# Kernel optimization log

Measured on AMD Instinct MI355X. Metric: run time of the kernel, lower is better.

The kernel has to match this reference:

```python
import jax, jax.numpy as jnp
import numpy as np

N_R, N_V, D, E_RR, L, G = 50000, 2000, 128, 800000, 3, 32


def setup_inputs() -> dict:
    key = jax.random.key(0)
    ks = jax.random.split(key, 10)
    x_real = jax.random.normal(ks[0], (N_R, D), dtype=jnp.float32)
    x_virtual = jax.random.normal(ks[1], (N_V, D), dtype=jnp.float32)
    # params: [num_layers, 3 relations (r_to_r, r_to_v, v_to_r), D, D]
    W_root = jax.random.normal(ks[2], (L, 3, D, D), dtype=jnp.float32) * 0.05
    W_nbr = jax.random.normal(ks[3], (L, 3, D, D), dtype=jnp.float32) * 0.05
    bias = jax.random.normal(ks[4], (L, 3, D), dtype=jnp.float32) * 0.05
    edge_rr = jax.random.randint(ks[5], (2, E_RR), 0, N_R)
    # one virtual-node edge per real node (hierarchical virtual nodes)
    src_rv = jnp.arange(N_R)
    dst_rv = jax.random.randint(ks[6], (N_R,), 0, N_V)
    edge_rv = jnp.stack([src_rv, dst_rv])          # real -> virtual
    edge_vr = jnp.stack([dst_rv, src_rv])          # virtual -> real
    batch_real = jnp.sort(jax.random.randint(ks[7], (N_R,), 0, G))
    return {
        "x_real": x_real, "x_virtual": x_virtual,
        "W_root": W_root, "W_nbr": W_nbr, "bias": bias,
        "edge_rr": edge_rr, "edge_rv": edge_rv, "edge_vr": edge_vr,
        "batch_real": batch_real,
    }


def _graph_conv(x_src, x_dst, src, dst, Wr, Wn, b, n_dst):
    # PyG GraphConv-style: root transform + sum-aggregated neighbor messages
    msg = jax.ops.segment_sum(x_src[src] @ Wn, dst, num_segments=n_dst)
    return x_dst @ Wr + msg + b


def _forward(x_real, x_virtual, W_root, W_nbr, bias, edge_rr, edge_rv, edge_vr, batch_real):
    x_r, x_v = x_real, x_virtual
    n_r, n_v = x_r.shape[0], x_v.shape[0]
    for l in range(W_root.shape[0]):
        # HeteroConv with aggr='sum': sum relation outputs per destination type
        c_rr = _graph_conv(x_r, x_r, edge_rr[0], edge_rr[1], W_root[l, 0], W_nbr[l, 0], bias[l, 0], n_r)
        c_vr = _graph_conv(x_v, x_r, edge_vr[0], edge_vr[1], W_root[l, 2], W_nbr[l, 2], bias[l, 2], n_r)
        c_rv = _graph_conv(x_r, x_v, edge_rv[0], edge_rv[1], W_root[l, 1], W_nbr[l, 1], bias[l, 1], n_v)
        # activation + dropout (eval mode -> identity)
        x_r = jax.nn.relu(c_rr + c_vr)
        x_v = jax.nn.relu(c_rv)
    # mean readout over real nodes per graph
    counts = jax.ops.segment_sum(jnp.ones((n_r,), x_r.dtype), batch_real, num_segments=G)
    graph_emb = jax.ops.segment_sum(x_r, batch_real, num_segments=G) / jnp.maximum(counts, 1.0)[:, None]
    return x_r, graph_emb


def reference(x_real, x_virtual, W_root, W_nbr, bias, edge_rr, edge_rv, edge_vr, batch_real):
    node_embedding, graph_embedding = _forward(
        x_real, x_virtual, W_root, W_nbr, bias, edge_rr, edge_rv, edge_vr, batch_real)
    return node_embedding, graph_embedding
```

## Files before the change

### kernel.cpp

```cpp
#include <hip/hip_runtime.h>
#include <hip/hip_bf16.h>

#define N_R   50000
#define N_V   2000
#define DIM   128
#define E_RR  800000
#define NLAY  3
#define NGR   32
#define RCHUNK 16

#define BUKD  128
#define NBUK  391
#define CHKE  2048
#define NCHK  391

typedef __attribute__((ext_vector_type(8))) short bf16x8;
typedef __attribute__((ext_vector_type(4))) float f32x4;
typedef __attribute__((ext_vector_type(8))) unsigned char u8x8;
typedef __attribute__((ext_vector_type(4))) unsigned char u8x4;

__device__ __forceinline__ ushort f2bf(float f) {
    unsigned u = __builtin_bit_cast(unsigned, f);
    unsigned r = (u + 0x7fffu + ((u >> 16) & 1u)) >> 16;
    return (ushort)r;
}
__device__ __forceinline__ float bf2f(ushort h) {
    unsigned u = ((unsigned)h) << 16;
    return __builtin_bit_cast(float, u);
}
__device__ __forceinline__ int lbound(const int* __restrict__ a, int n, int key) {
    int lo = 0, hi = n;
    while (lo < hi) { int mid = (lo + hi) >> 1; if (a[mid] < key) lo = mid + 1; else hi = mid; }
    return lo;
}

__global__ __launch_bounds__(256) void hist_kernel(
    const int* __restrict__ dst, int n, int* __restrict__ cnt)
{
    int i = blockIdx.x * 256 + threadIdx.x;
    if (i < n) atomicAdd(&cnt[dst[i]], 1);
}

__global__ __launch_bounds__(256) void scan_single_kernel(
    const int* __restrict__ cnt, int n, int nedges,
    int* __restrict__ rowptr, int* __restrict__ cursor)
{
    __shared__ int lds[256];
    __shared__ int carry;
    int t = threadIdx.x;
    if (t == 0) carry = 0;
    __syncthreads();
    for (int base = 0; base < n; base += 256) {
        int i = base + t;
        int v = (i < n) ? cnt[i] : 0;
        lds[t] = v;
        __syncthreads();
        #pragma unroll
        for (int off = 1; off < 256; off <<= 1) {
            int u = (t >= off) ? lds[t - off] : 0;
            __syncthreads();
            lds[t] += u;
            __syncthreads();
        }
        int excl = carry + lds[t] - v;
        if (i < n) {
            rowptr[i] = excl;
            if (cursor) cursor[i] = excl;
        }
        __syncthreads();
        if (t == 255) carry += lds[255];
        __syncthreads();
    }
    if (t == 0) rowptr[n] = nedges;
}

__global__ __launch_bounds__(256) void fill_kernel(
    const int* __restrict__ src, const int* __restrict__ dst, int n,
    int* __restrict__ cursor, int* __restrict__ col)
{
    int i = blockIdx.x * 256 + threadIdx.x;
    if (i < n) {
        int p = atomicAdd(&cursor[dst[i]], 1);
        col[p] = src[i];
    }
}

__global__ __launch_bounds__(256) void bkt_count_kernel(
    const int* __restrict__ dst, int* __restrict__ cnt2d)
{
    __shared__ int h[NBUK];
    int t = threadIdx.x, c = blockIdx.x;
    for (int i = t; i < NBUK; i += 256) h[i] = 0;
    __syncthreads();
    int e0 = c * CHKE, e1 = min(e0 + CHKE, E_RR);
    for (int e = e0 + t; e < e1; e += 256) atomicAdd(&h[dst[e] >> 7], 1);
    __syncthreads();
    for (int i = t; i < NBUK; i += 256) cnt2d[(size_t)c * NBUK + i] = h[i];
}

__global__ __launch_bounds__(64) void bkt_prefix_kernel(
    const int* __restrict__ cnt2d, int* __restrict__ rel2d, int* __restrict__ tot)
{
    int b = blockIdx.x, lane = threadIdx.x;
    int base = 0;
    for (int c0 = 0; c0 < NCHK; c0 += 64) {
        int c = c0 + lane;
        int v = (c < NCHK) ? cnt2d[(size_t)c * NBUK + b] : 0;
        int s = v;
        #pragma unroll
        for (int off = 1; off < 64; off <<= 1) {
            int u = __shfl_up(s, off);
            if (lane >= off) s += u;
        }
        if (c < NCHK) rel2d[(size_t)c * NBUK + b] = base + s - v;
        base += __shfl(s, 63);
    }
    if (lane == 0) tot[b] = base;
}

__global__ __launch_bounds__(256) void bkt_scatter_kernel(
    const int* __restrict__ src, const int* __restrict__ dst,
    const int* __restrict__ rel2d, const int* __restrict__ bstart,
    unsigned* __restrict__ ebuf)
{
    __shared__ int cur[NBUK];
    int t = threadIdx.x, c = blockIdx.x;
    for (int i = t; i < NBUK; i += 256)
        cur[i] = bstart[i] + rel2d[(size_t)c * NBUK + i];
    __syncthreads();
    int e0 = c * CHKE, e1 = min(e0 + CHKE, E_RR);
    for (int e = e0 + t; e < e1; e += 256) {
        int d = dst[e];
        int p = atomicAdd(&cur[d >> 7], 1);
        ebuf[p] = ((unsigned)d << 16) | (unsigned)src[e];
    }
}

__global__ __launch_bounds__(256) void bkt_fine_kernel(
    const unsigned* __restrict__ ebuf, const int* __restrict__ bstart,
    int* __restrict__ rowptr, int* __restrict__ col)
{
    __shared__ int cnt[BUKD];
    __shared__ int sc[BUKD];
    __shared__ int cur[BUKD];
    int b = blockIdx.x, t = threadIdx.x;
    int s0 = bstart[b], s1 = bstart[b + 1];
    if (t < BUKD) cnt[t] = 0;
    __syncthreads();
    for (int e = s0 + t; e < s1; e += 256)
        atomicAdd(&cnt[(ebuf[e] >> 16) & (BUKD - 1)], 1);
    __syncthreads();
    if (t < BUKD) sc[t] = cnt[t];
    __syncthreads();
    #pragma unroll
    for (int off = 1; off < BUKD; off <<= 1) {
        int v = (t < BUKD && t >= off) ? sc[t - off] : 0;
        __syncthreads();
        if (t < BUKD) sc[t] += v;
        __syncthreads();
    }
    if (t < BUKD) {
        int ex = sc[t] - cnt[t];
        int d = b * BUKD + t;
        if (d < N_R) rowptr[d] = s0 + ex;
        cur[t] = ex;
    }
    if (b == NBUK - 1 && t == 0) rowptr[N_R] = E_RR;
    __syncthreads();
    for (int e = s0 + t; e < s1; e += 256) {
        unsigned pk = ebuf[e];
        int p = atomicAdd(&cur[(pk >> 16) & (BUKD - 1)], 1);
        col[s0 + p] = (int)(pk & 0xffffu);
    }
}

__global__ __launch_bounds__(256) void quant_input_kernel(
    const float* __restrict__ in, unsigned char* __restrict__ q,
    float2* __restrict__ meta)
{
    int w = (blockIdx.x * 256 + threadIdx.x) >> 6;
    int lane = threadIdx.x & 63;
    if (w >= N_R) return;
    float2 v = *(const float2*)(in + (size_t)w * DIM + lane * 2);
    float mn = fminf(v.x, v.y), mx = fmaxf(v.x, v.y);
    #pragma unroll
    for (int off = 1; off < 64; off <<= 1) {
        mn = fminf(mn, __shfl_xor(mn, off));
        mx = fmaxf(mx, __shfl_xor(mx, off));
    }
    float range = mx - mn;
    float inv = (range > 0.f) ? 255.f / range : 0.f;
    unsigned q0 = (unsigned)__float2int_rn((v.x - mn) * inv);
    unsigned q1 = (unsigned)__float2int_rn((v.y - mn) * inv);
    *(ushort*)(q + (size_t)w * DIM + lane * 2) = (ushort)(q0 | (q1 << 8));
    if (lane == 0) meta[w] = make_float2(range / 255.f, mn);
}

__global__ __launch_bounds__(256) void build_wt_kernel(
    const float* __restrict__ Wroot, const float* __restrict__ Wnbr,
    ushort* __restrict__ WT)
{
    int idx = blockIdx.x * 256 + threadIdx.x;
    if (idx >= NLAY * DIM * 2 * DIM) return;
    int k = idx & 255;
    int n = (idx >> 8) & 127;
    int l = idx >> 15;
    float v;
    if (k < DIM) {
        const float* base = Wroot + (size_t)l * 3 * DIM * DIM;
        v = base[(size_t)k * DIM + n] + base[(size_t)(2 * DIM + k) * DIM + n];
    } else {
        v = Wnbr[((size_t)l * 3 * DIM + (k - DIM)) * DIM + n];
    }
    WT[idx] = f2bf(v);
}

__global__ __launch_bounds__(256) void combine_b_kernel(
    const float* __restrict__ bias, float* __restrict__ bc)
{
    int idx = blockIdx.x * 256 + threadIdx.x;
    if (idx >= NLAY * DIM) return;
    int l = idx / DIM;
    int rest = idx - l * DIM;
    const float* base = bias + (size_t)l * 3 * DIM;
    bc[idx] = base[rest] + base[2 * DIM + rest];
}

__global__ __launch_bounds__(128) void vlayer_kernel(
    const int* __restrict__ rowptr, const int* __restrict__ col,
    const unsigned char* __restrict__ Xq, const float2* __restrict__ Xm,
    const float* __restrict__ xv,
    const float* __restrict__ Wn2, const float* __restrict__ Wr1,
    const float* __restrict__ Wn1, const float* __restrict__ b1,
    float* __restrict__ Tv, float* __restrict__ xv_next, int doNext)
{
    __shared__ float arv_s[4 * DIM];
    int t = threadIdx.x;
    int lr = t >> 5;
    int j4 = (t & 31) << 2;
    int row = blockIdx.x * 4 + lr;

    if (doNext) {
        int beg = rowptr[row], end = rowptr[row + 1];
        float a0 = 0.f, a1 = 0.f, a2 = 0.f, a3 = 0.f, msum = 0.f;
        int e = beg;
        for (; e + 3 < end; e += 4) {
            int c0 = col[e + 0], c1 = col[e + 1], c2 = col[e + 2], c3 = col[e + 3];
            float2 m0 = Xm[c0], m1 = Xm[c1], m2 = Xm[c2], m3 = Xm[c3];
            u8x4 u0 = *(const u8x4*)(Xq + (size_t)c0 * DIM + j4);
            u8x4 u1 = *(const u8x4*)(Xq + (size_t)c1 * DIM + j4);
            u8x4 u2 = *(const u8x4*)(Xq + (size_t)c2 * DIM + j4);
            u8x4 u3 = *(const u8x4*)(Xq + (size_t)c3 * DIM + j4);
            a0 += m0.x * (float)u0[0] + m1.x * (float)u1[0] + m2.x * (float)u2[0] + m3.x * (float)u3[0];
            a1 += m0.x * (float)u0[1] + m1.x * (float)u1[1] + m2.x * (float)u2[1] + m3.x * (float)u3[1];
            a2 += m0.x * (float)u0[2] + m1.x * (float)u1[2] + m2.x * (float)u2[2] + m3.x * (float)u3[2];
            a3 += m0.x * (float)u0[3] + m1.x * (float)u1[3] + m2.x * (float)u2[3] + m3.x * (float)u3[3];
            msum += m0.y + m1.y + m2.y + m3.y;
        }
        for (; e < end; ++e) {
            int c0 = col[e];
            float2 m0 = Xm[c0];
            u8x4 u0 = *(const u8x4*)(Xq + (size_t)c0 * DIM + j4);
            a0 += m0.x * (float)u0[0];
            a1 += m0.x * (float)u0[1];
            a2 += m0.x * (float)u0[2];
            a3 += m0.x * (float)u0[3];
            msum += m0.y;
        }
        arv_s[lr * DIM + j4 + 0] = a0 + msum;
        arv_s[lr * DIM + j4 + 1] = a1 + msum;
        arv_s[lr * DIM + j4 + 2] = a2 + msum;
        arv_s[lr * DIM + j4 + 3] = a3 + msum;
        __syncthreads();
    }

    const float* arow = xv + (size_t)row * DIM;
    float4 tacc = make_float4(0.f, 0.f, 0.f, 0.f);
    float4 nacc = make_float4(0.f, 0.f, 0.f, 0.f);
    if (doNext) {
        #pragma unroll 4
        for (int k = 0; k < DIM; ++k) {
            float av = arow[k];
            float bv = arv_s[lr * DIM + k];
            float4 w2 = *(const float4*)(Wn2 + (size_t)k * DIM + j4);
            float4 wr = *(const float4*)(Wr1 + (size_t)k * DIM + j4);
            float4 wn = *(const float4*)(Wn1 + (size_t)k * DIM + j4);
            tacc.x += av * w2.x; tacc.y += av * w2.y;
            tacc.z += av * w2.z; tacc.w += av * w2.w;
            nacc.x += av * wr.x + bv * wn.x;
            nacc.y += av * wr.y + bv * wn.y;
            nacc.z += av * wr.z + bv * wn.z;
            nacc.w += av * wr.w + bv * wn.w;
        }
    } else {
        #pragma unroll 8
        for (int k = 0; k < DIM; ++k) {
            float av = arow[k];
            float4 w2 = *(const float4*)(Wn2 + (size_t)k * DIM + j4);
            tacc.x += av * w2.x; tacc.y += av * w2.y;
            tacc.z += av * w2.z; tacc.w += av * w2.w;
        }
    }
    *(float4*)(Tv + (size_t)row * DIM + j4) = tacc;
    if (doNext) {
        float4 b = *(const float4*)(b1 + j4);
        nacc.x = fmaxf(nacc.x + b.x, 0.f);
        nacc.y = fmaxf(nacc.y + b.y, 0.f);
        nacc.z = fmaxf(nacc.z + b.z, 0.f);
        nacc.w = fmaxf(nacc.w + b.w, 0.f);
        *(float4*)(xv_next + (size_t)row * DIM + j4) = nacc;
    }
}

__global__ __launch_bounds__(128) void fused_layer_kernel(
    const int* __restrict__ rowptr, const int* __restrict__ col,
    const unsigned char* __restrict__ Xq, const float2* __restrict__ Xm,
    const ushort* __restrict__ WT,
    const float* __restrict__ Tv,  const int* __restrict__ vmap,
    const float* __restrict__ bias,
    float* __restrict__ outF,
    unsigned char* __restrict__ Xq_out, float2* __restrict__ Xm_out, int M)
{
    __shared__ ushort a2[16 * DIM];
    __shared__ float ost[16 * DIM];
    int t = threadIdx.x;

    int wave = t >> 6, lane = t & 63;
    int rlo = lane & 15, hi = lane >> 4;
    int row0 = blockIdx.x * 16;
    int arowc = min(row0 + rlo, M - 1);
    float2 am = Xm[arowc];
    bf16x8 afr[8];
    #pragma unroll
    for (int j = 0; j < 4; ++j) {
        u8x8 uv = *(const u8x8*)(Xq + (size_t)arowc * DIM + 32 * j + 8 * hi);
        bf16x8 f;
        #pragma unroll
        for (int q = 0; q < 8; ++q)
            f[q] = (short)f2bf(am.x * (float)uv[q] + am.y);
        afr[j] = f;
    }
    int vr[4];
    #pragma unroll
    for (int i = 0; i < 4; ++i)
        vr[i] = vmap[min(row0 + 4 * hi + i, M - 1)];

    int g = t >> 4;
    int li = t & 15;
    for (int rr = g; rr < 16; rr += 8) {
        int drow = min(row0 + rr, M - 1);
        int beg = rowptr[drow], end = rowptr[drow + 1];
        float acc[8] = {0.f,0.f,0.f,0.f,0.f,0.f,0.f,0.f};
        float msum = 0.f;
        int e = beg;
        for (; e + 3 < end; e += 4) {
            int c0 = col[e + 0], c1 = col[e + 1], c2 = col[e + 2], c3 = col[e + 3];
            float2 m0 = Xm[c0], m1 = Xm[c1], m2 = Xm[c2], m3 = Xm[c3];
            u8x8 v0 = *(const u8x8*)(Xq + (size_t)c0 * DIM + li * 8);
            u8x8 v1 = *(const u8x8*)(Xq + (size_t)c1 * DIM + li * 8);
            u8x8 v2 = *(const u8x8*)(Xq + (size_t)c2 * DIM + li * 8);
            u8x8 v3 = *(const u8x8*)(Xq + (size_t)c3 * DIM + li * 8);
            #pragma unroll
            for (int q = 0; q < 8; ++q) {
                acc[q] += (m0.x * (float)v0[q] + m1.x * (float)v1[q])
                        + (m2.x * (float)v2[q] + m3.x * (float)v3[q]);
            }
            msum += (m0.y + m1.y) + (m2.y + m3.y);
        }
        for (; e < end; ++e) {
            int c0 = col[e];
            float2 m0 = Xm[c0];
            u8x8 v0 = *(const u8x8*)(Xq + (size_t)c0 * DIM + li * 8);
            #pragma unroll
            for (int q = 0; q < 8; ++q) acc[q] += m0.x * (float)v0[q];
            msum += m0.y;
        }
        bf16x8 pk;
        #pragma unroll
        for (int q = 0; q < 8; ++q) pk[q] = (short)f2bf(acc[q] + msum);
        int byte = rr * 256 + ((li * 16) ^ ((rr & 7) << 4));
        *(bf16x8*)((char*)a2 + byte) = pk;
    }
    __syncthreads();

    #pragma unroll
    for (int jj = 0; jj < 4; ++jj) {
        int byte = rlo * 256 + ((64 * jj + 16 * hi) ^ ((rlo & 7) << 4));
        afr[4 + jj] = *(const bf16x8*)((const char*)a2 + byte);
    }

    f32x4 acc[4];
    #pragma unroll
    for (int n = 0; n < 4; ++n) acc[n] = (f32x4){0.f, 0.f, 0.f, 0.f};

    #pragma unroll
    for (int n = 0; n < 4; ++n) {
        int nt = wave * 4 + n;
        const ushort* wrow = WT + (size_t)(nt * 16 + rlo) * (2 * DIM);
        #pragma unroll
        for (int j = 0; j < 8; ++j) {
            bf16x8 bfr = *(const bf16x8*)(wrow + 32 * j + 8 * hi);
            acc[n] = __builtin_amdgcn_mfma_f32_16x16x32_bf16(afr[j], bfr, acc[n], 0, 0, 0);
        }
    }

    if (outF) {
        #pragma unroll
        for (int n = 0; n < 4; ++n) {
            int ncol = (wave * 4 + n) * 16 + rlo;
            float bv = bias[ncol];
            #pragma unroll
            for (int i = 0; i < 4; ++i) {
                int orow = row0 + 4 * hi + i;
                if (orow >= M) continue;
                float v = acc[n][i] + bv + Tv[(size_t)vr[i] * DIM + ncol];
                outF[(size_t)orow * DIM + ncol] = fmaxf(v, 0.f);
            }
        }
    } else {
        #pragma unroll
        for (int n = 0; n < 4; ++n) {
            int ncol = (wave * 4 + n) * 16 + rlo;
            float bv = bias[ncol];
            #pragma unroll
            for (int i = 0; i < 4; ++i) {
                float v = acc[n][i] + bv + Tv[(size_t)vr[i] * DIM + ncol];
                ost[(4 * hi + i) * DIM + ncol] = fmaxf(v, 0.f);
            }
        }
        __syncthreads();
        for (int rr = g; rr < 16; rr += 8) {
            int orow = row0 + rr;
            float4 f0 = *(const float4*)(ost + rr * DIM + li * 8);
            float4 f1 = *(const float4*)(ost + rr * DIM + li * 8 + 4);
            float mn = fminf(fminf(fminf(f0.x, f0.y), fminf(f0.z, f0.w)),
                             fminf(fminf(f1.x, f1.y), fminf(f1.z, f1.w)));
            float mx = fmaxf(fmaxf(fmaxf(f0.x, f0.y), fmaxf(f0.z, f0.w)),
                             fmaxf(fmaxf(f1.x, f1.y), fmaxf(f1.z, f1.w)));
            #pragma unroll
            for (int off = 1; off < 16; off <<= 1) {
                mn = fminf(mn, __shfl_xor(mn, off, 16));
                mx = fmaxf(mx, __shfl_xor(mx, off, 16));
            }
            float range = mx - mn;
            float inv = (range > 0.f) ? 255.f / range : 0.f;
            if (orow < M) {
                u8x8 qv;
                qv[0] = (unsigned char)__float2int_rn((f0.x - mn) * inv);
                qv[1] = (unsigned char)__float2int_rn((f0.y - mn) * inv);
                qv[2] = (unsigned char)__float2int_rn((f0.z - mn) * inv);
                qv[3] = (unsigned char)__float2int_rn((f0.w - mn) * inv);
                qv[4] = (unsigned char)__float2int_rn((f1.x - mn) * inv);
                qv[5] = (unsigned char)__float2int_rn((f1.y - mn) * inv);
                qv[6] = (unsigned char)__float2int_rn((f1.z - mn) * inv);
                qv[7] = (unsigned char)__float2int_rn((f1.w - mn) * inv);
                *(u8x8*)(Xq_out + (size_t)orow * DIM + li * 8) = qv;
                if (li == 0) Xm_out[orow] = make_float2(range / 255.f, mn);
            }
        }
    }
}

__global__ __launch_bounds__(256) void readout_kernel(
    const float* __restrict__ xr, const int* __restrict__ batch,
    float* __restrict__ gsum, int nrows)
{
    __shared__ float lds[256 * 4];
    int g = blockIdx.x / RCHUNK;
    int chunk = blockIdx.x % RCHUNK;
    int lo = lbound(batch, nrows, g);
    int hi = lbound(batch, nrows, g + 1);
    int len = hi - lo;
    if (len == 0) return;
    int per = (len + RCHUNK - 1) / RCHUNK;
    int r0 = lo + chunk * per;
    int r1 = min(r0 + per, hi);

    int t = threadIdx.x;
    int c4 = (t & 31) << 2;
    int rsub = t >> 5;

    float4 acc = make_float4(0.f, 0.f, 0.f, 0.f);
    for (int r = r0 + rsub; r < r1; r += 8) {
        float4 v = *(const float4*)(xr + (size_t)r * DIM + c4);
        acc.x += v.x; acc.y += v.y; acc.z += v.z; acc.w += v.w;
    }
    *(float4*)(lds + t * 4) = acc;
    __syncthreads();
    if (rsub == 0) {
        float4 s = make_float4(0.f, 0.f, 0.f, 0.f);
        #pragma unroll
        for (int j = 0; j < 8; ++j) {
            float4 v = *(const float4*)(lds + (j * 32 + t) * 4);
            s.x += v.x; s.y += v.y; s.z += v.z; s.w += v.w;
        }
        atomicAdd(&gsum[(size_t)g * DIM + c4 + 0], s.x);
        atomicAdd(&gsum[(size_t)g * DIM + c4 + 1], s.y);
        atomicAdd(&gsum[(size_t)g * DIM + c4 + 2], s.z);
        atomicAdd(&gsum[(size_t)g * DIM + c4 + 3], s.w);
    }
}

__global__ __launch_bounds__(256) void finalize_kernel(
    const float* __restrict__ gsum, const int* __restrict__ batch,
    float* __restrict__ out, int nrows)
{
    int idx = blockIdx.x * 256 + threadIdx.x;
    if (idx >= NGR * DIM) return;
    int g = idx >> 7;
    int lo = lbound(batch, nrows, g);
    int hi = lbound(batch, nrows, g + 1);
    float c = fmaxf((float)(hi - lo), 1.f);
    out[idx] = gsum[idx] / c;
}

extern "C" void kernel_launch(void* const* d_in, const int* in_sizes, int n_in,
                              void* d_out, int out_size, void* d_ws, size_t ws_size,
                              hipStream_t stream)
{
    const float* x_real    = (const float*)d_in[0];
    const float* x_virtual = (const float*)d_in[1];
    const float* W_root    = (const float*)d_in[2];
    const float* W_nbr     = (const float*)d_in[3];
    const float* bias      = (const float*)d_in[4];
    const int*   edge_rr   = (const int*)d_in[5];
    const int*   edge_rv   = (const int*)d_in[6];
    const int*   edge_vr   = (const int*)d_in[7];
    const int*   batch     = (const int*)d_in[8];

    float* out = (float*)d_out;

    float2* meta0 = (float2*)d_ws;
    float2* meta1 = meta0 + N_R;
    float2* meta2 = meta1 + N_R;
    float*  Tv    = (float*)(meta2 + N_R);
    float*  xv_a  = Tv   + (size_t)N_V * DIM;
    float*  xv_b  = xv_a + (size_t)N_V * DIM;
    float*  bc    = xv_b + (size_t)N_V * DIM;
    float*  gsum  = bc   + (size_t)NLAY * DIM;
    ushort* WT    = (ushort*)(gsum + NGR * DIM);
    int* iws       = (int*)(WT + (size_t)NLAY * DIM * 2 * DIM);
    int* rowptr_rr = iws;
    int* col_rr    = rowptr_rr + N_R + 1;
    int* cnt_v     = col_rr + E_RR;
    int* rowptr_rv = cnt_v + N_V;
    int* cursor_rv = rowptr_rv + N_V + 1;
    int* col_rv    = cursor_rv + N_V;
    int* cnt2d     = col_rv + N_R;
    int* rel2d     = cnt2d + NCHK * NBUK;
    int* tot       = rel2d + NCHK * NBUK;
    int* bstart    = tot + NBUK;
    unsigned* ebuf = (unsigned*)(bstart + NBUK + 1);
    unsigned char* Q0 = (unsigned char*)(ebuf + E_RR);
    unsigned char* Q1 = Q0 + (size_t)N_R * DIM;
    unsigned char* Q2 = Q1 + (size_t)N_R * DIM;

    const int* rr_src = edge_rr;
    const int* rr_dst = edge_rr + E_RR;
    const int* rv_src = edge_rv;
    const int* rv_dst = edge_rv + N_R;

    bkt_count_kernel<<<NCHK, 256, 0, stream>>>(rr_dst, cnt2d);
    bkt_prefix_kernel<<<NBUK, 64, 0, stream>>>(cnt2d, rel2d, tot);
    scan_single_kernel<<<1, 256, 0, stream>>>(tot, NBUK, E_RR, bstart, nullptr);
    bkt_scatter_kernel<<<NCHK, 256, 0, stream>>>(rr_src, rr_dst, rel2d, bstart, ebuf);
    bkt_fine_kernel<<<NBUK, 256, 0, stream>>>(ebuf, bstart, rowptr_rr, col_rr);

    hipMemsetAsync(cnt_v, 0, (size_t)N_V * sizeof(int), stream);
    hist_kernel<<<(N_R + 255) / 256, 256, 0, stream>>>(rv_dst, N_R, cnt_v);
    scan_single_kernel<<<1, 256, 0, stream>>>(cnt_v, N_V, N_R, rowptr_rv, cursor_rv);
    fill_kernel<<<(N_R + 255) / 256, 256, 0, stream>>>(rv_src, rv_dst, N_R, cursor_rv, col_rv);

    build_wt_kernel<<<(NLAY * DIM * 2 * DIM + 255) / 256, 256, 0, stream>>>(W_root, W_nbr, WT);
    combine_b_kernel<<<(NLAY * DIM + 255) / 256, 256, 0, stream>>>(bias, bc);
    quant_input_kernel<<<(N_R * 64 + 255) / 256, 256, 0, stream>>>(x_real, Q0, meta0);

    unsigned char* Qcur = Q0;  float2* Mcur = meta0;
    const float* cur_xv = x_virtual;

    for (int l = 0; l < NLAY; ++l) {
        const float* Wn1 = W_nbr + ((size_t)l * 3 + 1) * DIM * DIM;
        const float* Wn2 = W_nbr + ((size_t)l * 3 + 2) * DIM * DIM;
        const float* Wr1 = W_root + ((size_t)l * 3 + 1) * DIM * DIM;
        const float* b1  = bias + ((size_t)l * 3 + 1) * DIM;

        int doNext = (l < NLAY - 1);
        float* xv_out = (l & 1) ? xv_b : xv_a;

        vlayer_kernel<<<N_V / 4, 128, 0, stream>>>(
            rowptr_rv, col_rv, Qcur, Mcur, cur_xv,
            Wn2, Wr1, Wn1, b1, Tv, xv_out, doNext);

        unsigned char* Qnext = (l == 0) ? Q1 : Q2;
        float2*        Mnext = (l == 0) ? meta1 : meta2;
        float* outF = (l == NLAY - 1) ? out : nullptr;
        fused_layer_kernel<<<(N_R + 15) / 16, 128, 0, stream>>>(
            rowptr_rr, col_rr, Qcur, Mcur, WT + (size_t)l * DIM * 2 * DIM,
            Tv, edge_vr, bc + (size_t)l * DIM,
            outF, outF ? nullptr : Qnext, outF ? nullptr : Mnext, N_R);

        if (doNext) { cur_xv = xv_out; Qcur = Qnext; Mcur = Mnext; }
    }

    hipMemsetAsync(gsum, 0, (size_t)NGR * DIM * sizeof(float), stream);
    readout_kernel<<<NGR * RCHUNK, 256, 0, stream>>>(out, batch, gsum, N_R);
    finalize_kernel<<<(NGR * DIM + 255) / 256, 256, 0, stream>>>(
        gsum, batch, out + (size_t)N_R * DIM, N_R);
}
```

Baseline: 375.3 us.

## Split quantized features into column-half planes and gather each half separately

Stores the uint8 node features as two 64-byte column planes instead of 128-byte rows, and moves the neighbor gather out of the fused layer kernel into two separate gather passes, one per half. Each pass touches a 3.2 MB plane that is more likely to stay in cache during random neighbor access. The gathered bf16 aggregate goes through a global buffer that the MFMA kernel then reads. This adds extra launches and a global write plus read of the 50000x128 bf16 aggregate each layer, and the features are now read twice.

```diff
diff --git a/kernel.cpp b/kernel.cpp
--- a/kernel.cpp
+++ b/kernel.cpp
@@ -19,6 +19,8 @@
 typedef __attribute__((ext_vector_type(8))) unsigned char u8x8;
 typedef __attribute__((ext_vector_type(4))) unsigned char u8x4;
 
+#define NR64 ((size_t)N_R * 64)
+
 __device__ __forceinline__ ushort f2bf(float f) {
     unsigned u = __builtin_bit_cast(unsigned, f);
     unsigned r = (u + 0x7fffu + ((u >> 16) & 1u)) >> 16;
@@ -192,7 +194,10 @@
     float inv = (range > 0.f) ? 255.f / range : 0.f;
     unsigned q0 = (unsigned)__float2int_rn((v.x - mn) * inv);
     unsigned q1 = (unsigned)__float2int_rn((v.y - mn) * inv);
-    *(ushort*)(q + (size_t)w * DIM + lane * 2) = (ushort)(q0 | (q1 << 8));
+    int plane = lane >> 5;
+    int off2 = (lane * 2) & 63;
+    *(ushort*)(q + (size_t)plane * NR64 + (size_t)w * 64 + off2)
+        = (ushort)(q0 | (q1 << 8));
     if (lane == 0) meta[w] = make_float2(range / 255.f, mn);
 }
 
@@ -226,6 +231,47 @@
     bc[idx] = base[rest] + base[2 * DIM + rest];
 }
 
+__global__ __launch_bounds__(256) void gather_half_kernel(
+    const int* __restrict__ rowptr, const int* __restrict__ col,
+    const unsigned char* __restrict__ XH,
+    const float2* __restrict__ Xm,
+    ushort* __restrict__ A2, int half, int nrows)
+{
+    int g = (blockIdx.x * 256 + threadIdx.x) >> 3;
+    int li = threadIdx.x & 7;
+    if (g >= nrows) return;
+    int beg = rowptr[g], end = rowptr[g + 1];
+    float acc[8] = {0.f,0.f,0.f,0.f,0.f,0.f,0.f,0.f};
+    float msum = 0.f;
+    int e = beg;
+    for (; e + 3 < end; e += 4) {
+        int c0 = col[e + 0], c1 = col[e + 1], c2 = col[e + 2], c3 = col[e + 3];
+        float2 m0 = Xm[c0], m1 = Xm[c1], m2 = Xm[c2], m3 = Xm[c3];
+        u8x8 v0 = *(const u8x8*)(XH + (size_t)c0 * 64 + li * 8);
+        u8x8 v1 = *(const u8x8*)(XH + (size_t)c1 * 64 + li * 8);
+        u8x8 v2 = *(const u8x8*)(XH + (size_t)c2 * 64 + li * 8);
+        u8x8 v3 = *(const u8x8*)(XH + (size_t)c3 * 64 + li * 8);
+        #pragma unroll
+        for (int q = 0; q < 8; ++q) {
+            acc[q] += (m0.x * (float)v0[q] + m1.x * (float)v1[q])
+                    + (m2.x * (float)v2[q] + m3.x * (float)v3[q]);
+        }
+        msum += (m0.y + m1.y) + (m2.y + m3.y);
+    }
+    for (; e < end; ++e) {
+        int c0 = col[e];
+        float2 m0 = Xm[c0];
+        u8x8 v0 = *(const u8x8*)(XH + (size_t)c0 * 64 + li * 8);
+        #pragma unroll
+        for (int q = 0; q < 8; ++q) acc[q] += m0.x * (float)v0[q];
+        msum += m0.y;
+    }
+    bf16x8 pk;
+    #pragma unroll
+    for (int q = 0; q < 8; ++q) pk[q] = (short)f2bf(acc[q] + msum);
+    *(bf16x8*)(A2 + (size_t)g * DIM + half * 64 + li * 8) = pk;
+}
+
 __global__ __launch_bounds__(128) void vlayer_kernel(
     const int* __restrict__ rowptr, const int* __restrict__ col,
     const unsigned char* __restrict__ Xq, const float2* __restrict__ Xm,
@@ -239,6 +285,8 @@
     int lr = t >> 5;
     int j4 = (t & 31) << 2;
     int row = blockIdx.x * 4 + lr;
+    const unsigned char* XP = Xq + (size_t)(j4 >> 6) * NR64;
+    int joff = j4 & 63;
 
     if (doNext) {
         int beg = rowptr[row], end = rowptr[row + 1];
@@ -247,10 +295,10 @@
         for (; e + 3 < end; e += 4) {
             int c0 = col[e + 0], c1 = col[e + 1], c2 = col[e + 2], c3 = col[e + 3];
             float2 m0 = Xm[c0], m1 = Xm[c1], m2 = Xm[c2], m3 = Xm[c3];
-            u8x4 u0 = *(const u8x4*)(Xq + (size_t)c0 * DIM + j4);
-            u8x4 u1 = *(const u8x4*)(Xq + (size_t)c1 * DIM + j4);
-            u8x4 u2 = *(const u8x4*)(Xq + (size_t)c2 * DIM + j4);
-            u8x4 u3 = *(const u8x4*)(Xq + (size_t)c3 * DIM + j4);
+            u8x4 u0 = *(const u8x4*)(XP + (size_t)c0 * 64 + joff);
+            u8x4 u1 = *(const u8x4*)(XP + (size_t)c1 * 64 + joff);
+            u8x4 u2 = *(const u8x4*)(XP + (size_t)c2 * 64 + joff);
+            u8x4 u3 = *(const u8x4*)(XP + (size_t)c3 * 64 + joff);
             a0 += m0.x * (float)u0[0] + m1.x * (float)u1[0] + m2.x * (float)u2[0] + m3.x * (float)u3[0];
             a1 += m0.x * (float)u0[1] + m1.x * (float)u1[1] + m2.x * (float)u2[1] + m3.x * (float)u3[1];
             a2 += m0.x * (float)u0[2] + m1.x * (float)u1[2] + m2.x * (float)u2[2] + m3.x * (float)u3[2];
@@ -260,7 +308,7 @@
         for (; e < end; ++e) {
             int c0 = col[e];
             float2 m0 = Xm[c0];
-            u8x4 u0 = *(const u8x4*)(Xq + (size_t)c0 * DIM + j4);
+            u8x4 u0 = *(const u8x4*)(XP + (size_t)c0 * 64 + joff);
             a0 += m0.x * (float)u0[0];
             a1 += m0.x * (float)u0[1];
             a2 += m0.x * (float)u0[2];
@@ -312,16 +360,14 @@
     }
 }
 
-__global__ __launch_bounds__(128) void fused_layer_kernel(
-    const int* __restrict__ rowptr, const int* __restrict__ col,
+__global__ __launch_bounds__(128) void mfma_layer_kernel(
     const unsigned char* __restrict__ Xq, const float2* __restrict__ Xm,
-    const ushort* __restrict__ WT,
+    const ushort* __restrict__ A2, const ushort* __restrict__ WT,
     const float* __restrict__ Tv,  const int* __restrict__ vmap,
     const float* __restrict__ bias,
     float* __restrict__ outF,
     unsigned char* __restrict__ Xq_out, float2* __restrict__ Xm_out, int M)
 {
-    __shared__ ushort a2[16 * DIM];
     __shared__ float ost[16 * DIM];
     int t = threadIdx.x;
 
@@ -333,61 +379,23 @@
     bf16x8 afr[8];
     #pragma unroll
     for (int j = 0; j < 4; ++j) {
-        u8x8 uv = *(const u8x8*)(Xq + (size_t)arowc * DIM + 32 * j + 8 * hi);
+        int k = 32 * j + 8 * hi;
+        const unsigned char* src = Xq + (size_t)(k >> 6) * NR64
+                                 + (size_t)arowc * 64 + (k & 63);
+        u8x8 uv = *(const u8x8*)src;
         bf16x8 f;
         #pragma unroll
         for (int q = 0; q < 8; ++q)
             f[q] = (short)f2bf(am.x * (float)uv[q] + am.y);
         afr[j] = f;
     }
+    #pragma unroll
+    for (int jj = 0; jj < 4; ++jj)
+        afr[4 + jj] = *(const bf16x8*)(A2 + (size_t)arowc * DIM + 32 * jj + 8 * hi);
     int vr[4];
     #pragma unroll
     for (int i = 0; i < 4; ++i)
         vr[i] = vmap[min(row0 + 4 * hi + i, M - 1)];
-
-    int g = t >> 4;
-    int li = t & 15;
-    for (int rr = g; rr < 16; rr += 8) {
-        int drow = min(row0 + rr, M - 1);
-        int beg = rowptr[drow], end = rowptr[drow + 1];
-        float acc[8] = {0.f,0.f,0.f,0.f,0.f,0.f,0.f,0.f};
-        float msum = 0.f;
-        int e = beg;
-        for (; e + 3 < end; e += 4) {
-            int c0 = col[e + 0], c1 = col[e + 1], c2 = col[e + 2], c3 = col[e + 3];
-            float2 m0 = Xm[c0], m1 = Xm[c1], m2 = Xm[c2], m3 = Xm[c3];
-            u8x8 v0 = *(const u8x8*)(Xq + (size_t)c0 * DIM + li * 8);
-            u8x8 v1 = *(const u8x8*)(Xq + (size_t)c1 * DIM + li * 8);
-            u8x8 v2 = *(const u8x8*)(Xq + (size_t)c2 * DIM + li * 8);
-            u8x8 v3 = *(const u8x8*)(Xq + (size_t)c3 * DIM + li * 8);
-            #pragma unroll
-            for (int q = 0; q < 8; ++q) {
-                acc[q] += (m0.x * (float)v0[q] + m1.x * (float)v1[q])
-                        + (m2.x * (float)v2[q] + m3.x * (float)v3[q]);
-            }
-            msum += (m0.y + m1.y) + (m2.y + m3.y);
-        }
-        for (; e < end; ++e) {
-            int c0 = col[e];
-            float2 m0 = Xm[c0];
-            u8x8 v0 = *(const u8x8*)(Xq + (size_t)c0 * DIM + li * 8);
-            #pragma unroll
-            for (int q = 0; q < 8; ++q) acc[q] += m0.x * (float)v0[q];
-            msum += m0.y;
-        }
-        bf16x8 pk;
-        #pragma unroll
-        for (int q = 0; q < 8; ++q) pk[q] = (short)f2bf(acc[q] + msum);
-        int byte = rr * 256 + ((li * 16) ^ ((rr & 7) << 4));
-        *(bf16x8*)((char*)a2 + byte) = pk;
-    }
-    __syncthreads();
-
-    #pragma unroll
-    for (int jj = 0; jj < 4; ++jj) {
-        int byte = rlo * 256 + ((64 * jj + 16 * hi) ^ ((rlo & 7) << 4));
-        afr[4 + jj] = *(const bf16x8*)((const char*)a2 + byte);
-    }
 
     f32x4 acc[4];
     #pragma unroll
@@ -429,6 +437,8 @@
             }
         }
         __syncthreads();
+        int g = t >> 4;
+        int li = t & 15;
         for (int rr = g; rr < 16; rr += 8) {
             int orow = row0 + rr;
             float4 f0 = *(const float4*)(ost + rr * DIM + li * 8);
@@ -454,7 +464,8 @@
                 qv[5] = (unsigned char)__float2int_rn((f1.y - mn) * inv);
                 qv[6] = (unsigned char)__float2int_rn((f1.z - mn) * inv);
                 qv[7] = (unsigned char)__float2int_rn((f1.w - mn) * inv);
-                *(u8x8*)(Xq_out + (size_t)orow * DIM + li * 8) = qv;
+                *(u8x8*)(Xq_out + (size_t)(li >> 3) * NR64
+                         + (size_t)orow * 64 + ((li * 8) & 63)) = qv;
                 if (li == 0) Xm_out[orow] = make_float2(range / 255.f, mn);
             }
         }
@@ -538,7 +549,8 @@
     float*  xv_b  = xv_a + (size_t)N_V * DIM;
     float*  bc    = xv_b + (size_t)N_V * DIM;
     float*  gsum  = bc   + (size_t)NLAY * DIM;
-    ushort* WT    = (ushort*)(gsum + NGR * DIM);
+    ushort* A2buf = (ushort*)(gsum + NGR * DIM);
+    ushort* WT    = A2buf + (size_t)N_R * DIM;
     int* iws       = (int*)(WT + (size_t)NLAY * DIM * 2 * DIM);
     int* rowptr_rr = iws;
     int* col_rr    = rowptr_rr + N_R + 1;
@@ -578,6 +590,8 @@
     unsigned char* Qcur = Q0;  float2* Mcur = meta0;
     const float* cur_xv = x_virtual;
 
+    const int gatherGrid = (N_R * 8 + 255) / 256;
+
     for (int l = 0; l < NLAY; ++l) {
         const float* Wn1 = W_nbr + ((size_t)l * 3 + 1) * DIM * DIM;
         const float* Wn2 = W_nbr + ((size_t)l * 3 + 2) * DIM * DIM;
@@ -591,11 +605,16 @@
             rowptr_rv, col_rv, Qcur, Mcur, cur_xv,
             Wn2, Wr1, Wn1, b1, Tv, xv_out, doNext);
 
+        gather_half_kernel<<<gatherGrid, 256, 0, stream>>>(
+            rowptr_rr, col_rr, Qcur,        Mcur, A2buf, 0, N_R);
+        gather_half_kernel<<<gatherGrid, 256, 0, stream>>>(
+            rowptr_rr, col_rr, Qcur + NR64, Mcur, A2buf, 1, N_R);
+
         unsigned char* Qnext = (l == 0) ? Q1 : Q2;
         float2*        Mnext = (l == 0) ? meta1 : meta2;
         float* outF = (l == NLAY - 1) ? out : nullptr;
-        fused_layer_kernel<<<(N_R + 15) / 16, 128, 0, stream>>>(
-            rowptr_rr, col_rr, Qcur, Mcur, WT + (size_t)l * DIM * 2 * DIM,
+        mfma_layer_kernel<<<(N_R + 15) / 16, 128, 0, stream>>>(
+            Qcur, Mcur, A2buf, WT + (size_t)l * DIM * 2 * DIM,
             Tv, edge_vr, bc + (size_t)l * DIM,
             outF, outF ? nullptr : Qnext, outF ? nullptr : Mnext, N_R);
 
```

Result: slower. 400.9 us (+6.8%).

## Remap virtual-node kernel to one block per virtual node with split edge gather

Applied to the files above, without the earlier changes.

The virtual-layer kernel now uses one 256-thread block per virtual node instead of four nodes per 128-thread block. The four waves split that node's incoming edges, and partial sums are reduced through shared memory. The two matvec products are then split across thread halves, so one half computes Tv and the other computes the next virtual features. This gives more parallelism for the roughly 25-edge gather per virtual node, at the cost of extra syncs, narrower uchar2 loads and scalar weight loads.

```diff
diff --git a/kernel.cpp b/kernel.cpp
--- a/kernel.cpp
+++ b/kernel.cpp
@@ -17,7 +17,6 @@
 typedef __attribute__((ext_vector_type(8))) short bf16x8;
 typedef __attribute__((ext_vector_type(4))) float f32x4;
 typedef __attribute__((ext_vector_type(8))) unsigned char u8x8;
-typedef __attribute__((ext_vector_type(4))) unsigned char u8x4;
 
 __device__ __forceinline__ ushort f2bf(float f) {
     unsigned u = __builtin_bit_cast(unsigned, f);
@@ -226,7 +225,7 @@
     bc[idx] = base[rest] + base[2 * DIM + rest];
 }
 
-__global__ __launch_bounds__(128) void vlayer_kernel(
+__global__ __launch_bounds__(256) void vlayer_kernel(
     const int* __restrict__ rowptr, const int* __restrict__ col,
     const unsigned char* __restrict__ Xq, const float2* __restrict__ Xm,
     const float* __restrict__ xv,
@@ -234,81 +233,46 @@
     const float* __restrict__ Wn1, const float* __restrict__ b1,
     float* __restrict__ Tv, float* __restrict__ xv_next, int doNext)
 {
-    __shared__ float arv_s[4 * DIM];
+    __shared__ float part[4 * DIM];
+    __shared__ float arv_s[DIM];
+    int v = blockIdx.x;
     int t = threadIdx.x;
-    int lr = t >> 5;
-    int j4 = (t & 31) << 2;
-    int row = blockIdx.x * 4 + lr;
+    int wave = t >> 6, lane = t & 63;
 
     if (doNext) {
-        int beg = rowptr[row], end = rowptr[row + 1];
-        float a0 = 0.f, a1 = 0.f, a2 = 0.f, a3 = 0.f, msum = 0.f;
-        int e = beg;
-        for (; e + 3 < end; e += 4) {
-            int c0 = col[e + 0], c1 = col[e + 1], c2 = col[e + 2], c3 = col[e + 3];
-            float2 m0 = Xm[c0], m1 = Xm[c1], m2 = Xm[c2], m3 = Xm[c3];
-            u8x4 u0 = *(const u8x4*)(Xq + (size_t)c0 * DIM + j4);
-            u8x4 u1 = *(const u8x4*)(Xq + (size_t)c1 * DIM + j4);
-            u8x4 u2 = *(const u8x4*)(Xq + (size_t)c2 * DIM + j4);
-            u8x4 u3 = *(const u8x4*)(Xq + (size_t)c3 * DIM + j4);
-            a0 += m0.x * (float)u0[0] + m1.x * (float)u1[0] + m2.x * (float)u2[0] + m3.x * (float)u3[0];
-            a1 += m0.x * (float)u0[1] + m1.x * (float)u1[1] + m2.x * (float)u2[1] + m3.x * (float)u3[1];
-            a2 += m0.x * (float)u0[2] + m1.x * (float)u1[2] + m2.x * (float)u2[2] + m3.x * (float)u3[2];
-            a3 += m0.x * (float)u0[3] + m1.x * (float)u1[3] + m2.x * (float)u2[3] + m3.x * (float)u3[3];
-            msum += m0.y + m1.y + m2.y + m3.y;
-        }
-        for (; e < end; ++e) {
-            int c0 = col[e];
-            float2 m0 = Xm[c0];
-            u8x4 u0 = *(const u8x4*)(Xq + (size_t)c0 * DIM + j4);
-            a0 += m0.x * (float)u0[0];
-            a1 += m0.x * (float)u0[1];
-            a2 += m0.x * (float)u0[2];
-            a3 += m0.x * (float)u0[3];
-            msum += m0.y;
-        }
-        arv_s[lr * DIM + j4 + 0] = a0 + msum;
-        arv_s[lr * DIM + j4 + 1] = a1 + msum;
-        arv_s[lr * DIM + j4 + 2] = a2 + msum;
-        arv_s[lr * DIM + j4 + 3] = a3 + msum;
-        __syncthreads();
-    }
-
-    const float* arow = xv + (size_t)row * DIM;
-    float4 tacc = make_float4(0.f, 0.f, 0.f, 0.f);
-    float4 nacc = make_float4(0.f, 0.f, 0.f, 0.f);
-    if (doNext) {
+        int beg = rowptr[v], end = rowptr[v + 1];
+        float a0 = 0.f, a1 = 0.f, msum = 0.f;
+        for (int e = beg + wave; e < end; e += 4) {
+            int c = col[e];
+            float2 m = Xm[c];
+            uchar2 u = *(const uchar2*)(Xq + (size_t)c * DIM + lane * 2);
+            a0 += m.x * (float)u.x;
+            a1 += m.x * (float)u.y;
+            msum += m.y;
+        }
+        part[wave * DIM + lane * 2 + 0] = a0 + msum;
+        part[wave * DIM + lane * 2 + 1] = a1 + msum;
+        __syncthreads();
+        if (t < DIM)
+            arv_s[t] = part[t] + part[DIM + t] + part[2 * DIM + t] + part[3 * DIM + t];
+        __syncthreads();
+    }
+
+    const float* arow = xv + (size_t)v * DIM;
+    if (t < DIM) {
+        float tacc = 0.f;
+        #pragma unroll 8
+        for (int k = 0; k < DIM; ++k)
+            tacc += arow[k] * Wn2[(size_t)k * DIM + t];
+        Tv[(size_t)v * DIM + t] = tacc;
+    } else if (doNext) {
+        int c = t - DIM;
+        float nacc = 0.f;
         #pragma unroll 4
-        for (int k = 0; k < DIM; ++k) {
-            float av = arow[k];
-            float bv = arv_s[lr * DIM + k];
-            float4 w2 = *(const float4*)(Wn2 + (size_t)k * DIM + j4);
-            float4 wr = *(const float4*)(Wr1 + (size_t)k * DIM + j4);
-            float4 wn = *(const float4*)(Wn1 + (size_t)k * DIM + j4);
-            tacc.x += av * w2.x; tacc.y += av * w2.y;
-            tacc.z += av * w2.z; tacc.w += av * w2.w;
-            nacc.x += av * wr.x + bv * wn.x;
-            nacc.y += av * wr.y + bv * wn.y;
-            nacc.z += av * wr.z + bv * wn.z;
-            nacc.w += av * wr.w + bv * wn.w;
-        }
-    } else {
-        #pragma unroll 8
-        for (int k = 0; k < DIM; ++k) {
-            float av = arow[k];
-            float4 w2 = *(const float4*)(Wn2 + (size_t)k * DIM + j4);
-            tacc.x += av * w2.x; tacc.y += av * w2.y;
-            tacc.z += av * w2.z; tacc.w += av * w2.w;
-        }
-    }
-    *(float4*)(Tv + (size_t)row * DIM + j4) = tacc;
-    if (doNext) {
-        float4 b = *(const float4*)(b1 + j4);
-        nacc.x = fmaxf(nacc.x + b.x, 0.f);
-        nacc.y = fmaxf(nacc.y + b.y, 0.f);
-        nacc.z = fmaxf(nacc.z + b.z, 0.f);
-        nacc.w = fmaxf(nacc.w + b.w, 0.f);
-        *(float4*)(xv_next + (size_t)row * DIM + j4) = nacc;
+        for (int k = 0; k < DIM; ++k)
+            nacc += arow[k] * Wr1[(size_t)k * DIM + c]
+                  + arv_s[k] * Wn1[(size_t)k * DIM + c];
+        xv_next[(size_t)v * DIM + c] = fmaxf(nacc + b1[c], 0.f);
     }
 }
 
@@ -587,7 +551,7 @@
         int doNext = (l < NLAY - 1);
         float* xv_out = (l & 1) ? xv_b : xv_a;
 
-        vlayer_kernel<<<N_V / 4, 128, 0, stream>>>(
+        vlayer_kernel<<<N_V, 256, 0, stream>>>(
             rowptr_rv, col_rv, Qcur, Mcur, cur_xv,
             Wn2, Wr1, Wn1, b1, Tv, xv_out, doNext);
 
```

Measured after the change: 341.3 us. 1.1x faster.
